# Kernel optimization log

Measured on AMD Instinct MI355X. Metric: run time of the kernel, lower is better.

Reference implementation:

```python
import jax, jax.numpy as jnp
import numpy as np

B, N, D = 8, 512, 512
H = 8
DK = D // H  # 64 per-channel attention maps


def setup_inputs() -> dict:
    key = jax.random.key(0)
    k1, k2, k3 = jax.random.split(key, 3)
    inputs = jax.random.normal(k1, (B, N, D), dtype=jnp.float32)
    W_qkv = jax.random.normal(k2, (D, 3 * DK), dtype=jnp.float32) * 0.02
    W_o = jax.random.normal(k3, (DK, D), dtype=jnp.float32) * 0.02
    return {"inputs": inputs, "W_qkv": W_qkv, "W_o": W_o}


def reference(inputs, W_qkv, W_o):
    d_k = W_qkv.shape[1] // 3
    QKV = inputs @ W_qkv                      # (B, N, 3*d_k)
    Q = QKV[:, :, 0 * d_k:1 * d_k]
    K = QKV[:, :, 1 * d_k:2 * d_k]
    V = QKV[:, :, 2 * d_k:3 * d_k]
    scale = 1.0 / jnp.sqrt(jnp.asarray(d_k, dtype=QKV.dtype))
    # per-channel (head_dim=1) attention, batched over the d_k channels
    S = jnp.einsum('bnc,bmc->bcnm', Q, K) * scale   # (B, d_k, N, N)
    A = jax.nn.softmax(S, axis=-1)
    SA = jnp.einsum('bcnm,bmc->bnc', A, V)          # (B, N, d_k)
    return SA @ W_o                                 # (B, N, D)
```

## Files before the change

kernel.cpp:

```cpp
#include <hip/hip_runtime.h>
#include <math.h>

#define BB 8
#define NN 512
#define DD 512
#define DKK 64
#define NC 192
#define CHN (BB * DKK * NN)
#define XEL (BB * NN * DD)
#define WEL (NC * DD)
#define WOEL (DKK * DD)
#define SAEL (BB * NN * DKK)
#define NFRAG_X (XEL / 8)
#define NFRAG_W (WEL / 8)
#define NFRAG_WO (WOEL / 8)
#define NJ 20

typedef short s8v   __attribute__((ext_vector_type(8)));
typedef float f32x4 __attribute__((ext_vector_type(4)));
typedef unsigned short ushort;

static __device__ __forceinline__ ushort bf16_rne(float f) {
    unsigned u = __float_as_uint(f);
    unsigned r = 0x7FFFu + ((u >> 16) & 1u);
    return (ushort)((u + r) >> 16);
}
static __device__ __forceinline__ float bf16_f32(ushort h) {
    return __uint_as_float(((unsigned)h) << 16);
}

__constant__ float c_invfact[NJ] = {
    1.0f, 1.0f, 0.5f, 1.6666667e-1f, 4.1666668e-2f, 8.3333338e-3f,
    1.3888889e-3f, 1.9841270e-4f, 2.4801588e-5f, 2.7557319e-6f,
    2.7557319e-7f, 2.5052108e-8f, 2.0876757e-9f, 1.6059044e-10f,
    1.1470746e-11f, 7.6471637e-13f, 4.7794773e-14f, 2.8114572e-15f,
    1.5619207e-16f, 8.2206352e-18f};

__global__ __launch_bounds__(256) void prep(const float* __restrict__ X,
                                            const float* __restrict__ W,
                                            const float* __restrict__ Wo,
                                            ushort* __restrict__ Xfh,
                                            ushort* __restrict__ Xfl,
                                            ushort* __restrict__ Wfh,
                                            ushort* __restrict__ Wfl,
                                            ushort* __restrict__ Woh,
                                            ushort* __restrict__ Wol) {
    const int gtid = blockIdx.x * 256 + threadIdx.x;
    if (gtid < NFRAG_X) {
        const int st   = gtid >> 10;
        const int ks   = (gtid >> 6) & 15;
        const int lane = gtid & 63;
        const int lm   = lane & 15;
        const int quad = lane >> 4;
        const int row  = st * 16 + lm;
        const int k0   = ks * 32 + quad * 8;
        const float4 xa = *(const float4*)(X + (size_t)row * DD + k0);
        const float4 xb = *(const float4*)(X + (size_t)row * DD + k0 + 4);
        const float xe[8] = {xa.x, xa.y, xa.z, xa.w, xb.x, xb.y, xb.z, xb.w};
        s8v h, l;
        #pragma unroll
        for (int e = 0; e < 8; ++e) {
            const ushort hh = bf16_rne(xe[e]);
            h[e] = (short)hh;
            l[e] = (short)bf16_rne(xe[e] - bf16_f32(hh));
        }
        *(s8v*)(Xfh + (size_t)gtid * 8) = h;
        *(s8v*)(Xfl + (size_t)gtid * 8) = l;
        return;
    }
    const int widx = gtid - NFRAG_X;
    if (widx < NFRAG_W) {
        const int ct   = widx >> 10;
        const int ks   = (widx >> 6) & 15;
        const int lane = widx & 63;
        const int lm   = lane & 15;
        const int quad = lane >> 4;
        const int chan = ct * 16 + lm;
        const int k0   = ks * 32 + quad * 8;
        s8v h, l;
        #pragma unroll
        for (int e = 0; e < 8; ++e) {
            const float w = W[(size_t)(k0 + e) * NC + chan];
            const ushort hh = bf16_rne(w);
            h[e] = (short)hh;
            l[e] = (short)bf16_rne(w - bf16_f32(hh));
        }
        *(s8v*)(Wfh + (size_t)widx * 8) = h;
        *(s8v*)(Wfl + (size_t)widx * 8) = l;
        return;
    }
    const int fi = widx - NFRAG_W;
    if (fi < NFRAG_WO) {
        const int lane = fi & 63;
        const int ks   = (fi >> 6) & 1;
        const int dt   = fi >> 7;
        const int lm   = lane & 15;
        const int quad = lane >> 4;
        const int d    = dt * 16 + lm;
        s8v h, l;
        #pragma unroll
        for (int e = 0; e < 8; ++e) {
            const int c = ks * 32 + quad * 8 + e;
            const float w = Wo[(size_t)c * DD + d];
            const ushort hh = bf16_rne(w);
            h[e] = (short)hh;
            l[e] = (short)bf16_rne(w - bf16_f32(hh));
        }
        *(s8v*)(Woh + (size_t)fi * 8) = h;
        *(s8v*)(Wol + (size_t)fi * 8) = l;
    }
}

__global__ __launch_bounds__(256) void qkv_mfma(const ushort* __restrict__ Xfh,
                                                const ushort* __restrict__ Xfl,
                                                const ushort* __restrict__ Wfh,
                                                const ushort* __restrict__ Wfl,
                                                float* __restrict__ qkv) {
    const int xcd  = blockIdx.x & 7;
    const int grp  = blockIdx.x >> 3;
    const int stl  = grp / 3;
    const int part = grp - stl * 3;
    const int st   = xcd * 32 + stl;
    const int ct   = part * 4 + (threadIdx.x >> 6);
    const int lane = threadIdx.x & 63;

    const ushort* ax_h = Xfh + ((size_t)(st * 16) * 64 + lane) * 8;
    const ushort* ax_l = Xfl + ((size_t)(st * 16) * 64 + lane) * 8;
    const ushort* bw_h = Wfh + ((size_t)(ct * 16) * 64 + lane) * 8;
    const ushort* bw_l = Wfl + ((size_t)(ct * 16) * 64 + lane) * 8;

    f32x4 acc = {0.f, 0.f, 0.f, 0.f};

    #pragma unroll 4
    for (int ks = 0; ks < 16; ++ks) {
        const size_t off = (size_t)ks * 512;
        const s8v ah = *(const s8v*)(ax_h + off);
        const s8v al = *(const s8v*)(ax_l + off);
        const s8v bh = *(const s8v*)(bw_h + off);
        const s8v bl = *(const s8v*)(bw_l + off);
        acc = __builtin_amdgcn_mfma_f32_16x16x32_bf16(ah, bh, acc, 0, 0, 0);
        acc = __builtin_amdgcn_mfma_f32_16x16x32_bf16(ah, bl, acc, 0, 0, 0);
        acc = __builtin_amdgcn_mfma_f32_16x16x32_bf16(al, bh, acc, 0, 0, 0);
    }

    const int lm    = lane & 15;
    const int quad  = lane >> 4;
    const int chan  = ct * 16 + lm;
    const int which = chan >> 6;
    const int c     = chan & 63;
    const int seq0  = st * 16 + quad * 4;
    const int b     = seq0 >> 9;
    const int n0    = seq0 & 511;
    const float4 v = {acc[0], acc[1], acc[2], acc[3]};
    *(float4*)(qkv + (size_t)which * CHN + ((size_t)(b * DKK + c)) * NN + n0) = v;
}

__global__ __launch_bounds__(256) void attn_taylor(const float* __restrict__ qkv,
                                                   ushort* __restrict__ SAh,
                                                   ushort* __restrict__ SAl) {
    __shared__ float red[4][2 * NJ];
    __shared__ float coef[2 * NJ];

    const int tid = threadIdx.x;
    const size_t chan = (size_t)blockIdx.x * NN;
    const float* qp = qkv + chan;
    const float* kp = qkv + CHN + chan;
    const float* vp = qkv + 2 * CHN + chan;

    const float k0 = kp[tid], k1 = kp[tid + 256];
    const float v0 = vp[tid], v1 = vp[tid + 256];

    float m[2 * NJ];
    float p0 = 1.f, p1 = 1.f;
    #pragma unroll
    for (int j = 0; j < NJ; ++j) {
        m[j]      = fmaf(p0, v0, p1 * v1);
        m[NJ + j] = p0 + p1;
        p0 *= k0;
        p1 *= k1;
    }

    #pragma unroll
    for (int j = 0; j < 2 * NJ; ++j) {
        float s = m[j];
        #pragma unroll
        for (int off = 32; off > 0; off >>= 1)
            s += __shfl_down(s, off, 64);
        m[j] = s;
    }
    if ((tid & 63) == 0) {
        #pragma unroll
        for (int j = 0; j < 2 * NJ; ++j) red[tid >> 6][j] = m[j];
    }
    __syncthreads();
    if (tid < 2 * NJ) {
        const int jj = (tid < NJ) ? tid : tid - NJ;
        coef[tid] = (red[0][tid] + red[1][tid] + red[2][tid] + red[3][tid]) *
                    c_invfact[jj];
    }
    __syncthreads();

    float c[2 * NJ];
    #pragma unroll
    for (int j = 0; j < 2 * NJ; ++j) c[j] = coef[j];

    const int b  = blockIdx.x >> 6;
    const int ch = blockIdx.x & 63;
    const int ks = ch >> 5;
    const int jf = ch & 7;
    const int lhi = ((ch & 31) >> 3) << 4;

    #pragma unroll
    for (int r = 0; r < 2; ++r) {
        const int n = tid + r * 256;
        const float t = qp[n] * 0.125f;
        float P = c[NJ - 1];
        float Q = c[2 * NJ - 1];
        #pragma unroll
        for (int j = NJ - 2; j >= 0; --j) {
            P = fmaf(P, t, c[j]);
            Q = fmaf(Q, t, c[NJ + j]);
        }
        const float val = P / Q;
        const ushort hi = bf16_rne(val);
        const ushort lo = bf16_rne(val - bf16_f32(hi));
        const int gseq = b * NN + n;
        const int st   = gseq >> 4;
        const int lane = lhi | (gseq & 15);
        const size_t addr = ((size_t)(st * 2 + ks) * 64 + lane) * 8 + jf;
        SAh[addr] = hi;
        SAl[addr] = lo;
    }
}

__global__ __launch_bounds__(256) void out_mfma(const ushort* __restrict__ SAh,
                                                const ushort* __restrict__ SAl,
                                                const ushort* __restrict__ Woh,
                                                const ushort* __restrict__ Wol,
                                                float* __restrict__ out) {
    const int widx = blockIdx.x * 4 + (threadIdx.x >> 6);
    const int st   = widx >> 3;
    const int dg   = widx & 7;
    const int lane = threadIdx.x & 63;

    const ushort* sa_h = SAh + ((size_t)(st * 2) * 64 + lane) * 8;
    const ushort* sa_l = SAl + ((size_t)(st * 2) * 64 + lane) * 8;
    const s8v ah0 = *(const s8v*)(sa_h);
    const s8v ah1 = *(const s8v*)(sa_h + 512);
    const s8v al0 = *(const s8v*)(sa_l);
    const s8v al1 = *(const s8v*)(sa_l + 512);

    const int lm   = lane & 15;
    const int quad = lane >> 4;
    const int seq0 = st * 16 + quad * 4;

    #pragma unroll
    for (int dti = 0; dti < 4; ++dti) {
        const int dt = dg * 4 + dti;
        const ushort* wo_h = Woh + ((size_t)(dt * 2) * 64 + lane) * 8;
        const ushort* wo_l = Wol + ((size_t)(dt * 2) * 64 + lane) * 8;
        const s8v bh0 = *(const s8v*)(wo_h);
        const s8v bh1 = *(const s8v*)(wo_h + 512);
        const s8v bl0 = *(const s8v*)(wo_l);
        const s8v bl1 = *(const s8v*)(wo_l + 512);

        f32x4 acc = {0.f, 0.f, 0.f, 0.f};
        acc = __builtin_amdgcn_mfma_f32_16x16x32_bf16(ah0, bh0, acc, 0, 0, 0);
        acc = __builtin_amdgcn_mfma_f32_16x16x32_bf16(ah0, bl0, acc, 0, 0, 0);
        acc = __builtin_amdgcn_mfma_f32_16x16x32_bf16(al0, bh0, acc, 0, 0, 0);
        acc = __builtin_amdgcn_mfma_f32_16x16x32_bf16(ah1, bh1, acc, 0, 0, 0);
        acc = __builtin_amdgcn_mfma_f32_16x16x32_bf16(ah1, bl1, acc, 0, 0, 0);
        acc = __builtin_amdgcn_mfma_f32_16x16x32_bf16(al1, bh1, acc, 0, 0, 0);

        const int d = dt * 16 + lm;
        #pragma unroll
        for (int r = 0; r < 4; ++r)
            out[(size_t)(seq0 + r) * DD + d] = acc[r];
    }
}

extern "C" void kernel_launch(void* const* d_in, const int* in_sizes, int n_in,
                              void* d_out, int out_size, void* d_ws, size_t ws_size,
                              hipStream_t stream) {
    const float* X    = (const float*)d_in[0];
    const float* Wqkv = (const float*)d_in[1];
    const float* Wo   = (const float*)d_in[2];
    float* out = (float*)d_out;

    float*  qkv = (float*)d_ws;
    ushort* Xfh = (ushort*)(qkv + (size_t)3 * CHN);
    ushort* Xfl = Xfh + (size_t)XEL;
    ushort* Wfh = Xfl + (size_t)XEL;
    ushort* Wfl = Wfh + (size_t)WEL;
    ushort* Woh = Wfl + (size_t)WEL;
    ushort* Wol = Woh + (size_t)WOEL;
    ushort* SAh = Wol + (size_t)WOEL;
    ushort* SAl = SAh + (size_t)SAEL;

    prep<<<dim3((NFRAG_X + NFRAG_W + NFRAG_WO) / 256), 256, 0, stream>>>(
        X, Wqkv, Wo, Xfh, Xfl, Wfh, Wfl, Woh, Wol);
    qkv_mfma<<<dim3(768), 256, 0, stream>>>(Xfh, Xfl, Wfh, Wfl, qkv);
    attn_taylor<<<dim3(BB * DKK), 256, 0, stream>>>(qkv, SAh, SAl);
    out_mfma<<<dim3(512), 256, 0, stream>>>(SAh, SAl, Woh, Wol, out);
}
```

Before: 89.16 us.

## Fuse bf16 split-precision prep into QKV and output GEMM kernels

Removes the separate prep kernel that converted X, W_qkv and W_o into hi/lo bf16 fragment buffers. The QKV kernel now loads a 16-row X tile into shared memory, splitting it on the fly, and converts W_qkv inside the k-loop. The output GEMM converts W_o directly from fp32. The hi/lo split now truncates instead of rounding to nearest, which trades some accuracy for fewer ALU ops. This drops one launch and the global round trip of the fragment buffers, but each block repeats the weight conversion and W_qkv is read with strided scalar loads.

```diff
diff --git a/kernel.cpp b/kernel.cpp
--- a/kernel.cpp
+++ b/kernel.cpp
@@ -7,26 +7,18 @@
 #define DKK 64
 #define NC 192
 #define CHN (BB * DKK * NN)
-#define XEL (BB * NN * DD)
-#define WEL (NC * DD)
-#define WOEL (DKK * DD)
 #define SAEL (BB * NN * DKK)
-#define NFRAG_X (XEL / 8)
-#define NFRAG_W (WEL / 8)
-#define NFRAG_WO (WOEL / 8)
 #define NJ 20
 
 typedef short s8v   __attribute__((ext_vector_type(8)));
 typedef float f32x4 __attribute__((ext_vector_type(4)));
 typedef unsigned short ushort;
 
-static __device__ __forceinline__ ushort bf16_rne(float f) {
-    unsigned u = __float_as_uint(f);
-    unsigned r = 0x7FFFu + ((u >> 16) & 1u);
-    return (ushort)((u + r) >> 16);
-}
-static __device__ __forceinline__ float bf16_f32(ushort h) {
-    return __uint_as_float(((unsigned)h) << 16);
+static __device__ __forceinline__ void split2(float w, ushort& h, ushort& l) {
+    const unsigned u = __float_as_uint(w);
+    h = (ushort)(u >> 16);
+    const float lo = w - __uint_as_float(u & 0xFFFF0000u);
+    l = (ushort)(__float_as_uint(lo) >> 16);
 }
 
 __constant__ float c_invfact[NJ] = {
@@ -36,116 +28,71 @@
     1.1470746e-11f, 7.6471637e-13f, 4.7794773e-14f, 2.8114572e-15f,
     1.5619207e-16f, 8.2206352e-18f};
 
-__global__ __launch_bounds__(256) void prep(const float* __restrict__ X,
-                                            const float* __restrict__ W,
-                                            const float* __restrict__ Wo,
-                                            ushort* __restrict__ Xfh,
-                                            ushort* __restrict__ Xfl,
-                                            ushort* __restrict__ Wfh,
-                                            ushort* __restrict__ Wfl,
-                                            ushort* __restrict__ Woh,
-                                            ushort* __restrict__ Wol) {
-    const int gtid = blockIdx.x * 256 + threadIdx.x;
-    if (gtid < NFRAG_X) {
-        const int st   = gtid >> 10;
-        const int ks   = (gtid >> 6) & 15;
-        const int lane = gtid & 63;
-        const int lm   = lane & 15;
-        const int quad = lane >> 4;
-        const int row  = st * 16 + lm;
-        const int k0   = ks * 32 + quad * 8;
-        const float4 xa = *(const float4*)(X + (size_t)row * DD + k0);
-        const float4 xb = *(const float4*)(X + (size_t)row * DD + k0 + 4);
-        const float xe[8] = {xa.x, xa.y, xa.z, xa.w, xb.x, xb.y, xb.z, xb.w};
-        s8v h, l;
-        #pragma unroll
-        for (int e = 0; e < 8; ++e) {
-            const ushort hh = bf16_rne(xe[e]);
-            h[e] = (short)hh;
-            l[e] = (short)bf16_rne(xe[e] - bf16_f32(hh));
-        }
-        *(s8v*)(Xfh + (size_t)gtid * 8) = h;
-        *(s8v*)(Xfl + (size_t)gtid * 8) = l;
-        return;
-    }
-    const int widx = gtid - NFRAG_X;
-    if (widx < NFRAG_W) {
-        const int ct   = widx >> 10;
-        const int ks   = (widx >> 6) & 15;
-        const int lane = widx & 63;
-        const int lm   = lane & 15;
-        const int quad = lane >> 4;
-        const int chan = ct * 16 + lm;
-        const int k0   = ks * 32 + quad * 8;
-        s8v h, l;
-        #pragma unroll
-        for (int e = 0; e < 8; ++e) {
-            const float w = W[(size_t)(k0 + e) * NC + chan];
-            const ushort hh = bf16_rne(w);
-            h[e] = (short)hh;
-            l[e] = (short)bf16_rne(w - bf16_f32(hh));
-        }
-        *(s8v*)(Wfh + (size_t)widx * 8) = h;
-        *(s8v*)(Wfl + (size_t)widx * 8) = l;
-        return;
-    }
-    const int fi = widx - NFRAG_W;
-    if (fi < NFRAG_WO) {
-        const int lane = fi & 63;
-        const int ks   = (fi >> 6) & 1;
-        const int dt   = fi >> 7;
-        const int lm   = lane & 15;
-        const int quad = lane >> 4;
-        const int d    = dt * 16 + lm;
-        s8v h, l;
-        #pragma unroll
-        for (int e = 0; e < 8; ++e) {
-            const int c = ks * 32 + quad * 8 + e;
-            const float w = Wo[(size_t)c * DD + d];
-            const ushort hh = bf16_rne(w);
-            h[e] = (short)hh;
-            l[e] = (short)bf16_rne(w - bf16_f32(hh));
-        }
-        *(s8v*)(Woh + (size_t)fi * 8) = h;
-        *(s8v*)(Wol + (size_t)fi * 8) = l;
-    }
-}
-
-__global__ __launch_bounds__(256) void qkv_mfma(const ushort* __restrict__ Xfh,
-                                                const ushort* __restrict__ Xfl,
-                                                const ushort* __restrict__ Wfh,
-                                                const ushort* __restrict__ Wfl,
-                                                float* __restrict__ qkv) {
+__global__ __launch_bounds__(256) void qkv_fused(const float* __restrict__ X,
+                                                 const float* __restrict__ W,
+                                                 float* __restrict__ qkv) {
+    __shared__ ushort Ah[16 * 512 + 128];
+    __shared__ ushort Al[16 * 512 + 128];
+
     const int xcd  = blockIdx.x & 7;
     const int grp  = blockIdx.x >> 3;
     const int stl  = grp / 3;
     const int part = grp - stl * 3;
     const int st   = xcd * 32 + stl;
-    const int ct   = part * 4 + (threadIdx.x >> 6);
-    const int lane = threadIdx.x & 63;
-
-    const ushort* ax_h = Xfh + ((size_t)(st * 16) * 64 + lane) * 8;
-    const ushort* ax_l = Xfl + ((size_t)(st * 16) * 64 + lane) * 8;
-    const ushort* bw_h = Wfh + ((size_t)(ct * 16) * 64 + lane) * 8;
-    const ushort* bw_l = Wfl + ((size_t)(ct * 16) * 64 + lane) * 8;
+    const int tid  = threadIdx.x;
+
+    #pragma unroll
+    for (int s = 0; s < 8; ++s) {
+        const int i   = tid + s * 256;
+        const int row = i >> 7;
+        const int k0  = (i & 127) * 4;
+        const float4 x = *(const float4*)(X + (size_t)(st * 16 + row) * DD + k0);
+        const float xe[4] = {x.x, x.y, x.z, x.w};
+        ushort h[4], l[4];
+        #pragma unroll
+        for (int e = 0; e < 4; ++e) split2(xe[e], h[e], l[e]);
+        const int ks   = k0 >> 5;
+        const int quad = (k0 >> 3) & 3;
+        const int e0   = k0 & 7;
+        const int lane = quad * 16 + row;
+        const size_t a = (size_t)(ks * 64 + lane) * 8 + e0 + ks * 8;
+        *(ushort4*)(Ah + a) = make_ushort4(h[0], h[1], h[2], h[3]);
+        *(ushort4*)(Al + a) = make_ushort4(l[0], l[1], l[2], l[3]);
+    }
+    __syncthreads();
+
+    const int wid  = tid >> 6;
+    const int ct   = part * 4 + wid;
+    const int lane = tid & 63;
+    const int lm   = lane & 15;
+    const int quad = lane >> 4;
+    const int chan = ct * 16 + lm;
 
     f32x4 acc = {0.f, 0.f, 0.f, 0.f};
 
     #pragma unroll 4
     for (int ks = 0; ks < 16; ++ks) {
-        const size_t off = (size_t)ks * 512;
-        const s8v ah = *(const s8v*)(ax_h + off);
-        const s8v al = *(const s8v*)(ax_l + off);
-        const s8v bh = *(const s8v*)(bw_h + off);
-        const s8v bl = *(const s8v*)(bw_l + off);
+        const int kb = ks * 32 + quad * 8;
+        float w[8];
+        #pragma unroll
+        for (int e = 0; e < 8; ++e)
+            w[e] = W[(size_t)(kb + e) * NC + chan];
+        s8v bh, bl;
+        #pragma unroll
+        for (int e = 0; e < 8; ++e) {
+            ushort hh, ll;
+            split2(w[e], hh, ll);
+            bh[e] = (short)hh;
+            bl[e] = (short)ll;
+        }
+        const size_t a = (size_t)(ks * 64 + lane) * 8 + ks * 8;
+        const s8v ah = *(const s8v*)(Ah + a);
+        const s8v al = *(const s8v*)(Al + a);
         acc = __builtin_amdgcn_mfma_f32_16x16x32_bf16(ah, bh, acc, 0, 0, 0);
         acc = __builtin_amdgcn_mfma_f32_16x16x32_bf16(ah, bl, acc, 0, 0, 0);
         acc = __builtin_amdgcn_mfma_f32_16x16x32_bf16(al, bh, acc, 0, 0, 0);
     }
 
-    const int lm    = lane & 15;
-    const int quad  = lane >> 4;
-    const int chan  = ct * 16 + lm;
     const int which = chan >> 6;
     const int c     = chan & 63;
     const int seq0  = st * 16 + quad * 4;
@@ -222,12 +169,12 @@
             Q = fmaf(Q, t, c[NJ + j]);
         }
         const float val = P / Q;
-        const ushort hi = bf16_rne(val);
-        const ushort lo = bf16_rne(val - bf16_f32(hi));
+        ushort hi, lo;
+        split2(val, hi, lo);
         const int gseq = b * NN + n;
-        const int st   = gseq >> 4;
+        const int stg  = gseq >> 4;
         const int lane = lhi | (gseq & 15);
-        const size_t addr = ((size_t)(st * 2 + ks) * 64 + lane) * 8 + jf;
+        const size_t addr = ((size_t)(stg * 2 + ks) * 64 + lane) * 8 + jf;
         SAh[addr] = hi;
         SAl[addr] = lo;
     }
@@ -235,13 +182,14 @@
 
 __global__ __launch_bounds__(256) void out_mfma(const ushort* __restrict__ SAh,
                                                 const ushort* __restrict__ SAl,
-                                                const ushort* __restrict__ Woh,
-                                                const ushort* __restrict__ Wol,
+                                                const float* __restrict__ Wo,
                                                 float* __restrict__ out) {
     const int widx = blockIdx.x * 4 + (threadIdx.x >> 6);
     const int st   = widx >> 3;
     const int dg   = widx & 7;
     const int lane = threadIdx.x & 63;
+    const int lm   = lane & 15;
+    const int quad = lane >> 4;
 
     const ushort* sa_h = SAh + ((size_t)(st * 2) * 64 + lane) * 8;
     const ushort* sa_l = SAl + ((size_t)(st * 2) * 64 + lane) * 8;
@@ -250,19 +198,22 @@
     const s8v al0 = *(const s8v*)(sa_l);
     const s8v al1 = *(const s8v*)(sa_l + 512);
 
-    const int lm   = lane & 15;
-    const int quad = lane >> 4;
     const int seq0 = st * 16 + quad * 4;
 
     #pragma unroll
     for (int dti = 0; dti < 4; ++dti) {
         const int dt = dg * 4 + dti;
-        const ushort* wo_h = Woh + ((size_t)(dt * 2) * 64 + lane) * 8;
-        const ushort* wo_l = Wol + ((size_t)(dt * 2) * 64 + lane) * 8;
-        const s8v bh0 = *(const s8v*)(wo_h);
-        const s8v bh1 = *(const s8v*)(wo_h + 512);
-        const s8v bl0 = *(const s8v*)(wo_l);
-        const s8v bl1 = *(const s8v*)(wo_l + 512);
+        const int d  = dt * 16 + lm;
+
+        s8v bh0, bl0, bh1, bl1;
+        #pragma unroll
+        for (int e = 0; e < 8; ++e) {
+            ushort hh, ll;
+            split2(Wo[(size_t)(quad * 8 + e) * DD + d], hh, ll);
+            bh0[e] = (short)hh;  bl0[e] = (short)ll;
+            split2(Wo[(size_t)(32 + quad * 8 + e) * DD + d], hh, ll);
+            bh1[e] = (short)hh;  bl1[e] = (short)ll;
+        }
 
         f32x4 acc = {0.f, 0.f, 0.f, 0.f};
         acc = __builtin_amdgcn_mfma_f32_16x16x32_bf16(ah0, bh0, acc, 0, 0, 0);
@@ -272,7 +223,6 @@
         acc = __builtin_amdgcn_mfma_f32_16x16x32_bf16(ah1, bl1, acc, 0, 0, 0);
         acc = __builtin_amdgcn_mfma_f32_16x16x32_bf16(al1, bh1, acc, 0, 0, 0);
 
-        const int d = dt * 16 + lm;
         #pragma unroll
         for (int r = 0; r < 4; ++r)
             out[(size_t)(seq0 + r) * DD + d] = acc[r];
@@ -288,18 +238,10 @@
     float* out = (float*)d_out;
 
     float*  qkv = (float*)d_ws;
-    ushort* Xfh = (ushort*)(qkv + (size_t)3 * CHN);
-    ushort* Xfl = Xfh + (size_t)XEL;
-    ushort* Wfh = Xfl + (size_t)XEL;
-    ushort* Wfl = Wfh + (size_t)WEL;
-    ushort* Woh = Wfl + (size_t)WEL;
-    ushort* Wol = Woh + (size_t)WOEL;
-    ushort* SAh = Wol + (size_t)WOEL;
+    ushort* SAh = (ushort*)(qkv + (size_t)3 * CHN);
     ushort* SAl = SAh + (size_t)SAEL;
 
-    prep<<<dim3((NFRAG_X + NFRAG_W + NFRAG_WO) / 256), 256, 0, stream>>>(
-        X, Wqkv, Wo, Xfh, Xfl, Wfh, Wfl, Woh, Wol);
-    qkv_mfma<<<dim3(768), 256, 0, stream>>>(Xfh, Xfl, Wfh, Wfl, qkv);
+    qkv_fused<<<dim3(768), 256, 0, stream>>>(X, Wqkv, qkv);
     attn_taylor<<<dim3(BB * DKK), 256, 0, stream>>>(qkv, SAh, SAl);
-    out_mfma<<<dim3(512), 256, 0, stream>>>(SAh, SAl, Woh, Wol, out);
-}
+    out_mfma<<<dim3(512), 256, 0, stream>>>(SAh, SAl, Wo, out);
+}
```

Result: faster. 84.85 us (-4.8%).
